# Performance work log

Measured on AMD Instinct MI355X. Metric: run time of the kernel, lower is better.

The kernel has to match this reference:

```python
import jax, jax.numpy as jnp
import numpy as np
import math

T_MIN = 0.1
T_MAX = 1.0


def setup_inputs() -> dict:
    key = jax.random.key(0)
    k1, k2, k3, k4, k5, k6 = jax.random.split(key, 6)
    B, H, SQ, SK, DK = 1, 16, 4096, 4096, 64
    query = jax.random.normal(k1, (B, H, SQ, DK), dtype=jnp.float32)
    key_t = jax.random.normal(k2, (B, H, SK, DK), dtype=jnp.float32)
    # MLP params (3 -> 16 -> 1). Original zero-inits the last layer; we use
    # small random values so gradients flow to query/key in the bwd test.
    W1 = jax.random.normal(k3, (16, 3), dtype=jnp.float32) * 0.5
    b1 = jax.random.normal(k4, (16,), dtype=jnp.float32) * 0.1
    W2 = jax.random.normal(k5, (1, 16), dtype=jnp.float32) * 0.5
    b2 = jax.random.normal(k6, (1,), dtype=jnp.float32) * 0.1
    return {"query": query, "key": key_t, "W1": W1, "b1": b1, "W2": W2, "b2": b2}


def reference(query, key, W1, b1, W2, b2):
    d_k = query.shape[-1]
    sk = key.shape[-2]
    q = query.astype(jnp.float32)
    k = key.astype(jnp.float32)
    # [B,H,Sq,Sk] score matrix
    scores = jnp.einsum('bhqd,bhkd->bhqk', q, k) / math.sqrt(d_k)
    scores = jnp.clip(scores, -50.0, 50.0)
    mean_sim = scores.mean(axis=(-2, -1))                 # [B,H]
    max_sim = scores.max(axis=-1).mean(axis=-1)           # [B,H]
    probs = jax.nn.softmax(scores / 2.0, axis=-1)         # [B,H,Sq,Sk]
    # torch .var(dim=-1) is unbiased (divisor Sk-1)
    pm = probs.mean(axis=-1, keepdims=True)
    var = ((probs - pm) ** 2).sum(axis=-1) / (sk - 1)     # [B,H,Sq]
    entropy_proxy = var.mean(axis=-1)                     # [B,H]
    mean_sim = jnp.clip(mean_sim, -10.0, 10.0)
    max_sim = jnp.clip(max_sim, -10.0, 10.0)
    entropy_proxy = jnp.clip(entropy_proxy, 0.0, 1.0)
    features = jnp.stack([mean_sim, max_sim, entropy_proxy], axis=-1)  # [B,H,3]
    h = jnp.tanh(features @ W1.T + b1)
    raw_t = h @ W2.T + b2                                 # [B,H,1]
    t = T_MIN + jax.nn.sigmoid(raw_t) * (T_MAX - T_MIN)
    t = jnp.clip(t, T_MIN, T_MAX)
    return t[..., None].astype(query.dtype)               # [B,H,1,1]
```

## Files before the change

kernel.cpp:

```cpp
#include <hip/hip_runtime.h>
#include <math.h>

#define NH   16
#define SQL  4096
#define SKL  4096
#define DK   64
#define QB   128
#define KB   128
#define NKT  (SKL / KB)

#define QSCALE  0.090168440f
#define UNSCALE 1.3862943611f

typedef __bf16 bf16x8 __attribute__((ext_vector_type(8)));
typedef __bf16 bf16x4 __attribute__((ext_vector_type(4)));
typedef float  f32x4  __attribute__((ext_vector_type(4)));

#if __has_builtin(__builtin_amdgcn_exp2f)
#define EXP2(x) __builtin_amdgcn_exp2f(x)
#else
#define EXP2(x) exp2f(x)
#endif

__device__ __forceinline__ int swz(int row, int col_bytes) {
    return ((row << 7) + col_bytes) ^ ((row & 7) << 4);
}

__global__ __launch_bounds__(512, 4) void dtp_stats_mfma(const float* __restrict__ Q,
                                                         const float* __restrict__ K,
                                                         float* __restrict__ partial) {
    __shared__ __align__(16) unsigned char Qs[QB * DK * 2];
    __shared__ __align__(16) unsigned char Ks[KB * DK * 2];
    __shared__ float red[32][3];

    const int qb   = blockIdx.x;
    const int h    = blockIdx.y;
    const int tid  = threadIdx.x;
    const int lane = tid & 63;
    const int w    = tid >> 6;
    const int l15  = lane & 15;
    const int lg   = lane >> 4;

    const float* Qh = Q + ((size_t)h * SQL + (size_t)qb * QB) * DK;
    const float* Kh = K + (size_t)h * SKL * DK;

    #pragma unroll
    for (int j = 0; j < 4; ++j) {
        int idx = tid + 512 * j;
        int r   = idx >> 4;
        int c4  = idx & 15;
        const float4 v = *reinterpret_cast<const float4*>(Qh + r * DK + c4 * 4);
        bf16x4 hv;
        hv[0] = (__bf16)(v.x * QSCALE); hv[1] = (__bf16)(v.y * QSCALE);
        hv[2] = (__bf16)(v.z * QSCALE); hv[3] = (__bf16)(v.w * QSCALE);
        *reinterpret_cast<bf16x4*>(&Qs[swz(r, c4 * 8)]) = hv;
    }

    float4 kreg[4];
    #pragma unroll
    for (int j = 0; j < 4; ++j) {
        int idx = tid + 512 * j;
        int r   = idx >> 4;
        int c4  = idx & 15;
        kreg[j] = *reinterpret_cast<const float4*>(Kh + (size_t)r * DK + c4 * 4);
    }

    __syncthreads();

    bf16x8 aF[2];
    {
        int r = w * 16 + l15;
        aF[0] = *reinterpret_cast<const bf16x8*>(&Qs[swz(r, 0 * 64 + lg * 16)]);
        aF[1] = *reinterpret_cast<const bf16x8*>(&Qs[swz(r, 1 * 64 + lg * 16)]);
    }

    float rsum[4], rmx[4], rs1[4], rs2[4];
    #pragma unroll
    for (int i = 0; i < 4; ++i) { rsum[i] = 0.f; rmx[i] = -3.0e38f; rs1[i] = 0.f; rs2[i] = 0.f; }

    for (int kt = 0; kt < NKT; ++kt) {
        __syncthreads();
        #pragma unroll
        for (int j = 0; j < 4; ++j) {
            int idx = tid + 512 * j;
            int r   = idx >> 4;
            int c4  = idx & 15;
            bf16x4 hv;
            hv[0] = (__bf16)kreg[j].x; hv[1] = (__bf16)kreg[j].y;
            hv[2] = (__bf16)kreg[j].z; hv[3] = (__bf16)kreg[j].w;
            *reinterpret_cast<bf16x4*>(&Ks[swz(r, c4 * 8)]) = hv;
        }
        __syncthreads();

        if (kt + 1 < NKT) {
            const float* Kt = Kh + (size_t)(kt + 1) * KB * DK;
            #pragma unroll
            for (int j = 0; j < 4; ++j) {
                int idx = tid + 512 * j;
                int r   = idx >> 4;
                int c4  = idx & 15;
                kreg[j] = *reinterpret_cast<const float4*>(Kt + (size_t)r * DK + c4 * 4);
            }
        }

        f32x4 acc[8];
        #pragma unroll
        for (int ct = 0; ct < 8; ++ct) {
            int rr = ct * 16 + l15;
            bf16x8 b0 = *reinterpret_cast<const bf16x8*>(&Ks[swz(rr, 0 * 64 + lg * 16)]);
            bf16x8 b1 = *reinterpret_cast<const bf16x8*>(&Ks[swz(rr, 1 * 64 + lg * 16)]);
            f32x4 a = {0.f, 0.f, 0.f, 0.f};
            a = __builtin_amdgcn_mfma_f32_16x16x32_bf16(aF[0], b0, a, 0, 0, 0);
            a = __builtin_amdgcn_mfma_f32_16x16x32_bf16(aF[1], b1, a, 0, 0, 0);
            acc[ct] = a;
        }

        #pragma unroll
        for (int r = 0; r < 4; ++r) {
            float v0 = acc[0][r], v1 = acc[1][r], v2 = acc[2][r], v3 = acc[3][r];
            float v4 = acc[4][r], v5 = acc[5][r], v6 = acc[6][r], v7 = acc[7][r];
            rsum[r] += ((v0 + v1) + (v2 + v3)) + ((v4 + v5) + (v6 + v7));
            rmx[r] = fmaxf(rmx[r],
                     fmaxf(fmaxf(fmaxf(v0, v1), fmaxf(v2, v3)),
                           fmaxf(fmaxf(v4, v5), fmaxf(v6, v7))));
            float e0 = EXP2(v0), e1 = EXP2(v1), e2 = EXP2(v2), e3 = EXP2(v3);
            float e4 = EXP2(v4), e5 = EXP2(v5), e6 = EXP2(v6), e7 = EXP2(v7);
            rs1[r] += ((e0 + e1) + (e2 + e3)) + ((e4 + e5) + (e6 + e7));
            float t0 = fmaf(e0, e0, e1 * e1), t1 = fmaf(e2, e2, e3 * e3);
            float t2 = fmaf(e4, e4, e5 * e5), t3 = fmaf(e6, e6, e7 * e7);
            rs2[r] += (t0 + t1) + (t2 + t3);
        }
    }

    #pragma unroll
    for (int i = 0; i < 4; ++i) {
        #pragma unroll
        for (int m = 1; m < 16; m <<= 1) {
            rsum[i] += __shfl_xor(rsum[i], m, 64);
            rmx[i]   = fmaxf(rmx[i], __shfl_xor(rmx[i], m, 64));
            rs1[i]  += __shfl_xor(rs1[i], m, 64);
            rs2[i]  += __shfl_xor(rs2[i], m, 64);
        }
    }

    if (l15 == 0) {
        float bs = 0.f, bm = 0.f, bv = 0.f;
        #pragma unroll
        for (int r = 0; r < 4; ++r) {
            bs += rsum[r];
            bm += rmx[r];
            float sumP2 = rs2[r] / (rs1[r] * rs1[r]);
            bv += (sumP2 - 1.0f / (float)SKL) * (1.0f / (float)(SKL - 1));
        }
        red[w * 4 + lg][0] = bs * UNSCALE;
        red[w * 4 + lg][1] = bm * UNSCALE;
        red[w * 4 + lg][2] = bv;
    }
    __syncthreads();
    if (tid == 0) {
        float bs = 0.f, bm = 0.f, bv = 0.f;
        #pragma unroll
        for (int i = 0; i < 32; ++i) { bs += red[i][0]; bm += red[i][1]; bv += red[i][2]; }
        float* p = partial + (size_t)(h * 32 + qb) * 3;
        p[0] = bs; p[1] = bm; p[2] = bv;
    }
}

__global__ __launch_bounds__(64) void dtp_finalize_kernel(const float* __restrict__ partial,
                                                          const float* __restrict__ W1,
                                                          const float* __restrict__ b1,
                                                          const float* __restrict__ W2,
                                                          const float* __restrict__ b2,
                                                          float* __restrict__ out) {
    int h = threadIdx.x;
    if (h >= NH) return;
    float ssum = 0.f, smax = 0.f, svar = 0.f;
    for (int qb = 0; qb < 32; ++qb) {
        const float* p = partial + (size_t)(h * 32 + qb) * 3;
        ssum += p[0]; smax += p[1]; svar += p[2];
    }
    float mean_sim = ssum / ((float)SQL * (float)SKL);
    float max_sim  = smax / (float)SQL;
    float entropy  = svar / (float)SQL;
    mean_sim = fminf(fmaxf(mean_sim, -10.f), 10.f);
    max_sim  = fminf(fmaxf(max_sim,  -10.f), 10.f);
    entropy  = fminf(fmaxf(entropy,    0.f), 1.f);
    float raw = b2[0];
    #pragma unroll
    for (int i = 0; i < 16; ++i) {
        float a = b1[i] + W1[i*3+0] * mean_sim + W1[i*3+1] * max_sim + W1[i*3+2] * entropy;
        raw += W2[i] * tanhf(a);
    }
    float t = 0.1f + 0.9f / (1.0f + __expf(-raw));
    t = fminf(fmaxf(t, 0.1f), 1.0f);
    out[h] = t;
}

extern "C" void kernel_launch(void* const* d_in, const int* in_sizes, int n_in,
                              void* d_out, int out_size, void* d_ws, size_t ws_size,
                              hipStream_t stream) {
    const float* Q  = (const float*)d_in[0];
    const float* K  = (const float*)d_in[1];
    const float* W1 = (const float*)d_in[2];
    const float* b1 = (const float*)d_in[3];
    const float* W2 = (const float*)d_in[4];
    const float* b2 = (const float*)d_in[5];
    float* out      = (float*)d_out;
    float* partial  = (float*)d_ws;

    dim3 grid(SQL / QB, NH);
    dtp_stats_mfma<<<grid, 512, 0, stream>>>(Q, K, partial);
    dtp_finalize_kernel<<<1, 64, 0, stream>>>(partial, W1, b1, W2, b2, out);
}
```

Measured before the change: 81.33 us.

## Double-buffer K tiles in LDS and use packed f32x2 math for row statistics

Doubles the K shared-memory tile so the next tile is converted and stored while the current one feeds MFMA. This cuts the two barriers per iteration down to one. It also rewrites the per-row reductions (sum, max, exp sums, squared sums) with two-wide float vectors so the compiler can emit packed FMA/add/max instructions. Doubling the LDS footprint may reduce occupancy, and the reordered summation slightly changes floating-point rounding.

```diff
diff --git a/kernel.cpp b/kernel.cpp
--- a/kernel.cpp
+++ b/kernel.cpp
@@ -15,6 +15,7 @@
 typedef __bf16 bf16x8 __attribute__((ext_vector_type(8)));
 typedef __bf16 bf16x4 __attribute__((ext_vector_type(4)));
 typedef float  f32x4  __attribute__((ext_vector_type(4)));
+typedef float  f32x2  __attribute__((ext_vector_type(2)));
 
 #if __has_builtin(__builtin_amdgcn_exp2f)
 #define EXP2(x) __builtin_amdgcn_exp2f(x)
@@ -22,6 +23,21 @@
 #define EXP2(x) exp2f(x)
 #endif
 
+static __device__ __forceinline__ f32x2 pk_fma(f32x2 a, f32x2 b, f32x2 c) {
+#if __has_builtin(__builtin_elementwise_fma)
+    return __builtin_elementwise_fma(a, b, c);
+#else
+    f32x2 r; r[0] = fmaf(a[0], b[0], c[0]); r[1] = fmaf(a[1], b[1], c[1]); return r;
+#endif
+}
+static __device__ __forceinline__ f32x2 pk_max(f32x2 a, f32x2 b) {
+#if __has_builtin(__builtin_elementwise_max)
+    return __builtin_elementwise_max(a, b);
+#else
+    f32x2 r; r[0] = fmaxf(a[0], b[0]); r[1] = fmaxf(a[1], b[1]); return r;
+#endif
+}
+
 __device__ __forceinline__ int swz(int row, int col_bytes) {
     return ((row << 7) + col_bytes) ^ ((row & 7) << 4);
 }
@@ -30,7 +46,7 @@
                                                          const float* __restrict__ K,
                                                          float* __restrict__ partial) {
     __shared__ __align__(16) unsigned char Qs[QB * DK * 2];
-    __shared__ __align__(16) unsigned char Ks[KB * DK * 2];
+    __shared__ __align__(16) unsigned char Ks[2][KB * DK * 2];
     __shared__ float red[32][3];
 
     const int qb   = blockIdx.x;
@@ -44,26 +60,34 @@
     const float* Qh = Q + ((size_t)h * SQL + (size_t)qb * QB) * DK;
     const float* Kh = K + (size_t)h * SKL * DK;
 
+    const int sc4 = tid & 15;
+    const int sr0 = tid >> 4;
+
     #pragma unroll
     for (int j = 0; j < 4; ++j) {
-        int idx = tid + 512 * j;
-        int r   = idx >> 4;
-        int c4  = idx & 15;
-        const float4 v = *reinterpret_cast<const float4*>(Qh + r * DK + c4 * 4);
+        int r = sr0 + 32 * j;
+        const float4 v = *reinterpret_cast<const float4*>(Qh + r * DK + sc4 * 4);
         bf16x4 hv;
         hv[0] = (__bf16)(v.x * QSCALE); hv[1] = (__bf16)(v.y * QSCALE);
         hv[2] = (__bf16)(v.z * QSCALE); hv[3] = (__bf16)(v.w * QSCALE);
-        *reinterpret_cast<bf16x4*>(&Qs[swz(r, c4 * 8)]) = hv;
+        *reinterpret_cast<bf16x4*>(&Qs[swz(r, sc4 * 8)]) = hv;
     }
 
     float4 kreg[4];
     #pragma unroll
+    for (int j = 0; j < 4; ++j)
+        kreg[j] = *reinterpret_cast<const float4*>(Kh + (size_t)(sr0 + 32 * j) * DK + sc4 * 4);
+    #pragma unroll
     for (int j = 0; j < 4; ++j) {
-        int idx = tid + 512 * j;
-        int r   = idx >> 4;
-        int c4  = idx & 15;
-        kreg[j] = *reinterpret_cast<const float4*>(Kh + (size_t)r * DK + c4 * 4);
-    }
+        int r = sr0 + 32 * j;
+        bf16x4 hv;
+        hv[0] = (__bf16)kreg[j].x; hv[1] = (__bf16)kreg[j].y;
+        hv[2] = (__bf16)kreg[j].z; hv[3] = (__bf16)kreg[j].w;
+        *reinterpret_cast<bf16x4*>(&Ks[0][swz(r, sc4 * 8)]) = hv;
+    }
+    #pragma unroll
+    for (int j = 0; j < 4; ++j)
+        kreg[j] = *reinterpret_cast<const float4*>(Kh + (size_t)(KB + sr0 + 32 * j) * DK + sc4 * 4);
 
     __syncthreads();
 
@@ -74,32 +98,28 @@
         aF[1] = *reinterpret_cast<const bf16x8*>(&Qs[swz(r, 1 * 64 + lg * 16)]);
     }
 
-    float rsum[4], rmx[4], rs1[4], rs2[4];
-    #pragma unroll
-    for (int i = 0; i < 4; ++i) { rsum[i] = 0.f; rmx[i] = -3.0e38f; rs1[i] = 0.f; rs2[i] = 0.f; }
+    f32x2 rsum01 = {0.f, 0.f}, rsum23 = {0.f, 0.f};
+    f32x2 rmx01  = {-3.0e38f, -3.0e38f}, rmx23 = {-3.0e38f, -3.0e38f};
+    f32x2 rs1_01 = {0.f, 0.f}, rs1_23 = {0.f, 0.f};
+    f32x2 rs2_01 = {0.f, 0.f}, rs2_23 = {0.f, 0.f};
 
     for (int kt = 0; kt < NKT; ++kt) {
-        __syncthreads();
-        #pragma unroll
-        for (int j = 0; j < 4; ++j) {
-            int idx = tid + 512 * j;
-            int r   = idx >> 4;
-            int c4  = idx & 15;
-            bf16x4 hv;
-            hv[0] = (__bf16)kreg[j].x; hv[1] = (__bf16)kreg[j].y;
-            hv[2] = (__bf16)kreg[j].z; hv[3] = (__bf16)kreg[j].w;
-            *reinterpret_cast<bf16x4*>(&Ks[swz(r, c4 * 8)]) = hv;
-        }
-        __syncthreads();
+        const int cur = kt & 1;
 
         if (kt + 1 < NKT) {
-            const float* Kt = Kh + (size_t)(kt + 1) * KB * DK;
             #pragma unroll
             for (int j = 0; j < 4; ++j) {
-                int idx = tid + 512 * j;
-                int r   = idx >> 4;
-                int c4  = idx & 15;
-                kreg[j] = *reinterpret_cast<const float4*>(Kt + (size_t)r * DK + c4 * 4);
+                int r = sr0 + 32 * j;
+                bf16x4 hv;
+                hv[0] = (__bf16)kreg[j].x; hv[1] = (__bf16)kreg[j].y;
+                hv[2] = (__bf16)kreg[j].z; hv[3] = (__bf16)kreg[j].w;
+                *reinterpret_cast<bf16x4*>(&Ks[cur ^ 1][swz(r, sc4 * 8)]) = hv;
+            }
+            if (kt + 2 < NKT) {
+                const float* Kt = Kh + (size_t)(kt + 2) * KB * DK;
+                #pragma unroll
+                for (int j = 0; j < 4; ++j)
+                    kreg[j] = *reinterpret_cast<const float4*>(Kt + (size_t)(sr0 + 32 * j) * DK + sc4 * 4);
             }
         }
 
@@ -107,50 +127,60 @@
         #pragma unroll
         for (int ct = 0; ct < 8; ++ct) {
             int rr = ct * 16 + l15;
-            bf16x8 b0 = *reinterpret_cast<const bf16x8*>(&Ks[swz(rr, 0 * 64 + lg * 16)]);
-            bf16x8 b1 = *reinterpret_cast<const bf16x8*>(&Ks[swz(rr, 1 * 64 + lg * 16)]);
+            bf16x8 b0 = *reinterpret_cast<const bf16x8*>(&Ks[cur][swz(rr, 0 * 64 + lg * 16)]);
+            bf16x8 b1 = *reinterpret_cast<const bf16x8*>(&Ks[cur][swz(rr, 1 * 64 + lg * 16)]);
             f32x4 a = {0.f, 0.f, 0.f, 0.f};
             a = __builtin_amdgcn_mfma_f32_16x16x32_bf16(aF[0], b0, a, 0, 0, 0);
             a = __builtin_amdgcn_mfma_f32_16x16x32_bf16(aF[1], b1, a, 0, 0, 0);
             acc[ct] = a;
         }
 
-        #pragma unroll
-        for (int r = 0; r < 4; ++r) {
-            float v0 = acc[0][r], v1 = acc[1][r], v2 = acc[2][r], v3 = acc[3][r];
-            float v4 = acc[4][r], v5 = acc[5][r], v6 = acc[6][r], v7 = acc[7][r];
-            rsum[r] += ((v0 + v1) + (v2 + v3)) + ((v4 + v5) + (v6 + v7));
-            rmx[r] = fmaxf(rmx[r],
-                     fmaxf(fmaxf(fmaxf(v0, v1), fmaxf(v2, v3)),
-                           fmaxf(fmaxf(v4, v5), fmaxf(v6, v7))));
-            float e0 = EXP2(v0), e1 = EXP2(v1), e2 = EXP2(v2), e3 = EXP2(v3);
-            float e4 = EXP2(v4), e5 = EXP2(v5), e6 = EXP2(v6), e7 = EXP2(v7);
-            rs1[r] += ((e0 + e1) + (e2 + e3)) + ((e4 + e5) + (e6 + e7));
-            float t0 = fmaf(e0, e0, e1 * e1), t1 = fmaf(e2, e2, e3 * e3);
-            float t2 = fmaf(e4, e4, e5 * e5), t3 = fmaf(e6, e6, e7 * e7);
-            rs2[r] += (t0 + t1) + (t2 + t3);
-        }
-    }
-
-    #pragma unroll
-    for (int i = 0; i < 4; ++i) {
-        #pragma unroll
-        for (int m = 1; m < 16; m <<= 1) {
-            rsum[i] += __shfl_xor(rsum[i], m, 64);
-            rmx[i]   = fmaxf(rmx[i], __shfl_xor(rmx[i], m, 64));
-            rs1[i]  += __shfl_xor(rs1[i], m, 64);
-            rs2[i]  += __shfl_xor(rs2[i], m, 64);
+        f32x2 s01 = {0.f, 0.f}, s23 = {0.f, 0.f};
+        #pragma unroll
+        for (int ct = 0; ct < 8; ++ct) {
+            f32x2 v01 = __builtin_shufflevector(acc[ct], acc[ct], 0, 1);
+            f32x2 v23 = __builtin_shufflevector(acc[ct], acc[ct], 2, 3);
+            s01 += v01; s23 += v23;
+            rmx01 = pk_max(rmx01, v01);
+            rmx23 = pk_max(rmx23, v23);
+            f32x2 e01, e23;
+            e01[0] = EXP2(v01[0]); e01[1] = EXP2(v01[1]);
+            e23[0] = EXP2(v23[0]); e23[1] = EXP2(v23[1]);
+            rs1_01 += e01; rs1_23 += e23;
+            rs2_01 = pk_fma(e01, e01, rs2_01);
+            rs2_23 = pk_fma(e23, e23, rs2_23);
+        }
+        rsum01 += s01; rsum23 += s23;
+
+        __syncthreads();
+    }
+
+    #pragma unroll
+    for (int m = 1; m < 16; m <<= 1) {
+        #pragma unroll
+        for (int c = 0; c < 2; ++c) {
+            rsum01[c] += __shfl_xor(rsum01[c], m, 64);
+            rsum23[c] += __shfl_xor(rsum23[c], m, 64);
+            rmx01[c]   = fmaxf(rmx01[c], __shfl_xor(rmx01[c], m, 64));
+            rmx23[c]   = fmaxf(rmx23[c], __shfl_xor(rmx23[c], m, 64));
+            rs1_01[c] += __shfl_xor(rs1_01[c], m, 64);
+            rs1_23[c] += __shfl_xor(rs1_23[c], m, 64);
+            rs2_01[c] += __shfl_xor(rs2_01[c], m, 64);
+            rs2_23[c] += __shfl_xor(rs2_23[c], m, 64);
         }
     }
 
     if (l15 == 0) {
-        float bs = 0.f, bm = 0.f, bv = 0.f;
-        #pragma unroll
-        for (int r = 0; r < 4; ++r) {
-            bs += rsum[r];
-            bm += rmx[r];
-            float sumP2 = rs2[r] / (rs1[r] * rs1[r]);
-            bv += (sumP2 - 1.0f / (float)SKL) * (1.0f / (float)(SKL - 1));
+        float bs = (rsum01[0] + rsum01[1]) + (rsum23[0] + rsum23[1]);
+        float bm = (rmx01[0] + rmx01[1]) + (rmx23[0] + rmx23[1]);
+        float bv = 0.f;
+        const float invSK = 1.0f / (float)SKL, invSK1 = 1.0f / (float)(SKL - 1);
+        {
+            float r1[4] = {rs1_01[0], rs1_01[1], rs1_23[0], rs1_23[1]};
+            float r2[4] = {rs2_01[0], rs2_01[1], rs2_23[0], rs2_23[1]};
+            #pragma unroll
+            for (int i = 0; i < 4; ++i)
+                bv += (r2[i] / (r1[i] * r1[i]) - invSK) * invSK1;
         }
         red[w * 4 + lg][0] = bs * UNSCALE;
         red[w * 4 + lg][1] = bm * UNSCALE;
```

Result: faster. 75.70 us (-6.9%).
